# Kernel optimization log

Hardware: AMD Instinct MI355X
Metric: run time of the kernel (lower is better)

Reference implementation:

```python
import jax, jax.numpy as jnp
import numpy as np

D_MODEL = 256
N_FEATURES = 32768
N_BLOCKS = 8
MIN_FEATURES = 512
BATCH = 2048
ALPHA = 0.99          # RunningAvgNormalizer alpha
EPS_CTRL = 3e-4       # L1RegController eps
TARGET_L0 = 100.0


def _pareto_seg(n_features, n_blocks, min_features, rng):
    # mirrors get_pareto_block_bounds, returning per-feature block ids
    cdf = 1.0 - (np.arange(n_features - min_features + 1) / (n_features - min_features + 1)) ** 0.5
    pdf = np.concatenate([np.zeros(min_features), np.abs(cdf[1:] - cdf[:-1])])
    pdf = pdf / pdf.sum()
    sp = np.sort(rng.choice(n_features, size=n_blocks - 1, replace=False, p=pdf))
    return np.searchsorted(sp, np.arange(n_features), side='right').astype(np.int32)


def setup_inputs() -> dict:
    key = jax.random.key(0)
    k0, k1 = jax.random.split(key, 2)
    x = jax.random.normal(k0, (BATCH, D_MODEL), jnp.float32)
    W_enc = jax.random.normal(k1, (D_MODEL, N_FEATURES), jnp.float32) / np.sqrt(D_MODEL)
    b_enc = -0.04 * jnp.ones((N_FEATURES,), jnp.float32)
    W_dec = (0.1 * W_enc / jnp.linalg.norm(W_enc, axis=0, keepdims=True)).T
    b_dec = jnp.zeros((D_MODEL,), jnp.float32)
    bw = np.arange(1, N_BLOCKS + 1, dtype=np.float32) ** 1.0  # block_weight_power = 1.0
    block_weights = jnp.asarray(bw / bw.max())
    running_avg = jnp.asarray([np.sqrt(D_MODEL)], jnp.float32)  # warmed-up running norm
    l1_scale = jnp.ones((1,), jnp.float32)
    seg = jnp.asarray(_pareto_seg(N_FEATURES, N_BLOCKS, MIN_FEATURES, np.random.default_rng(0)))
    return {"x": x, "W_enc": W_enc, "b_enc": b_enc, "W_dec": W_dec, "b_dec": b_dec,
            "block_weights": block_weights, "running_avg": running_avg,
            "l1_scale": l1_scale, "seg": seg}


def reference(x, W_enc, b_enc, W_dec, b_dec, block_weights, running_avg, l1_scale, seg):
    K = block_weights.shape[0]
    B, d = x.shape
    # RunningAvgNormalizer.normalize(update=True): update EMA, then scale (no grad through EMA)
    ra = ALPHA * running_avg[0] + (1.0 - ALPHA) * jnp.mean(jnp.linalg.norm(x, axis=-1))
    ra = jax.lax.stop_gradient(ra)
    xn = x * (jnp.sqrt(jnp.float32(d)) / ra)
    acts = jax.nn.relu(xn @ W_enc + b_enc)                       # [B, F]
    Wd_norms = jnp.linalg.norm(W_dec, axis=1)                    # [F]
    # per-block log-loss: sum over block features of mean-over-batch log term
    per_feat = jnp.mean(jnp.log(acts * Wd_norms + 0.1) - jnp.log(0.1), axis=0)  # [F]
    block_l1 = jax.ops.segment_sum(per_feat, seg, num_segments=K)               # [K]
    l1_loss = jnp.mean(block_weights * jnp.cumsum(block_l1))
    # per-block decode: (acts masked to block) @ W_dec, sequential over K small blocks
    onehot = (seg[None, :] == jnp.arange(K)[:, None]).astype(acts.dtype)  # [K, F]
    block_preds = jax.lax.map(lambda m: (acts * m) @ W_dec, onehot)       # [K, B, d]
    cum_preds = jnp.cumsum(block_preds, axis=0) + b_dec                   # b_dec added to preds[0] pre-cumsum
    block_errs = jnp.mean(jnp.sum((cum_preds - xn[None]) ** 2, axis=-1), axis=-1) * block_weights
    mse_loss = jnp.mean(block_errs)
    # L1RegController (no-grad)
    avg_l0 = jax.lax.stop_gradient(jnp.sum(acts > 0).astype(jnp.float32) / B)
    l1_reg_scale = jnp.where(avg_l0 < TARGET_L0, l1_scale[0] * (1.0 - EPS_CTRL), l1_scale[0] * (1.0 + EPS_CTRL))
    loss = mse_loss + l1_reg_scale * l1_loss
    return loss
```

## Files before the change

kernel.cpp:

```cpp
#include <hip/hip_runtime.h>

typedef float  f32x4  __attribute__((ext_vector_type(4)));
typedef __bf16 bf16x8 __attribute__((ext_vector_type(8)));
typedef __bf16 bf16x4 __attribute__((ext_vector_type(4)));
typedef unsigned short u16;

#define BATCH 2048
#define DM    256
#define NFEAT 32768
#define NBLK  8
#define ALPHA_C   0.99f
#define EPS_CTRL  3e-4f
#define TARGET_L0 100.0f

#define BT    32
#define FC    2048
#define NCHUNK (NFEAT / FC)
#define MACRO 128
#define NMACRO (FC / MACRO)
#define NPMAX 24
#define ACTS_SZ (BT * MACRO)

#define WS_RA    0
#define WS_SCALE 1
#define WS_L0    2
#define WS_L1    4
#define WS_ERR   16
#define WSI_BND  32
#define WSI_PTN  40
#define WSI_PTS  41
#define WSI_PSEG 66
#define WS_WDN   256
#define PIECES_OFF_BYTES ((size_t)262144)
#define PIECES_BYTES ((size_t)NPMAX * BATCH * DM * 2)
#define WEP_OFF_BYTES (PIECES_OFF_BYTES + PIECES_BYTES)
#define WDP_OFF_BYTES (WEP_OFF_BYTES + (size_t)NFEAT * DM * 2)

#define RAW_BARRIER() asm volatile("s_waitcnt lgkmcnt(0)\n\ts_barrier" ::: "memory")

static __device__ inline u16 f2b(float f) {
    return __builtin_bit_cast(u16, (__bf16)f);
}
static __device__ inline float b2f(u16 u) {
    return (float)__builtin_bit_cast(__bf16, u);
}
static __device__ inline f32x4 mfma16(bf16x8 a, bf16x8 b, f32x4 c) {
    return __builtin_amdgcn_mfma_f32_16x16x32_bf16(a, b, c, 0, 0, 0);
}

__global__ __launch_bounds__(256) void k_prep(const float* __restrict__ x,
                                              const float* __restrict__ Wd,
                                              const int* __restrict__ seg,
                                              float* ws) {
    const int bid = blockIdx.x;
    const int wave = threadIdx.x >> 6, lane = threadIdx.x & 63;
    if (bid < NFEAT / 4) {
        const int f = bid * 4 + wave;
        const float4 v = *reinterpret_cast<const float4*>(Wd + (size_t)f * DM + lane * 4);
        float s = v.x * v.x + v.y * v.y + v.z * v.z + v.w * v.w;
        #pragma unroll
        for (int o = 32; o; o >>= 1) s += __shfl_xor(s, o);
        if (lane == 0) ws[WS_WDN + f] = sqrtf(s);
    } else if (bid < NFEAT / 4 + BATCH / 4) {
        const int row = (bid - NFEAT / 4) * 4 + wave;
        const float4 v = *reinterpret_cast<const float4*>(x + (size_t)row * DM + lane * 4);
        float s = v.x * v.x + v.y * v.y + v.z * v.z + v.w * v.w;
        #pragma unroll
        for (int o = 32; o; o >>= 1) s += __shfl_xor(s, o);
        if (lane == 0) atomicAdd(&ws[WS_RA], sqrtf(s));
    } else {
        const int f = (bid - NFEAT / 4 - BATCH / 4) * 256 + threadIdx.x;
        if (f > 0 && f < NFEAT) {
            const int s = seg[f];
            if (s != seg[f - 1]) ((int*)ws)[WSI_BND + s] = f;
        }
    }
}

__global__ void k_pt2(const int* __restrict__ seg,
                      const float* __restrict__ ravg, float* ws) {
    __shared__ int stv[NCHUNK + NBLK];
    __shared__ int outL[NPMAX];
    __shared__ int NL;
    int* wsi = (int*)ws;
    const int t = threadIdx.x;
    if (t < NCHUNK) stv[t] = t * FC;
    else if (t < NCHUNK + NBLK - 1) stv[t] = wsi[WSI_BND + (t - NCHUNK + 1)];
    __syncthreads();
    if (t == 0) {
        int i = 0, j = NCHUNK, N = 0;
        while (i < NCHUNK || j < NCHUNK + NBLK - 1) {
            int v;
            if (i < NCHUNK && (j >= NCHUNK + NBLK - 1 || stv[i] <= stv[j])) v = stv[i++];
            else v = stv[j++];
            if (N == 0 || outL[N - 1] != v) outL[N++] = v;
        }
        NL = N;
    }
    __syncthreads();
    const int N = NL;
    if (t < N) {
        wsi[WSI_PTS + t] = outL[t];
        wsi[WSI_PSEG + t] = seg[outL[t]];
    }
    if (t == 0) {
        wsi[WSI_PTN] = N;
        wsi[WSI_PTS + N] = NFEAT;
        float ra = ALPHA_C * ravg[0] + (1.0f - ALPHA_C) * (ws[WS_RA] / (float)BATCH);
        ws[WS_SCALE] = 16.0f / ra;
    }
}

__global__ __launch_bounds__(256) void k_pack(const float* __restrict__ We,
                                              const float* __restrict__ Wd,
                                              u16* __restrict__ WeP,
                                              u16* __restrict__ WdP) {
    const int bid = blockIdx.x;
    if (bid < 4096) {
        const int tid = bid * 256 + threadIdx.x;
        const int l = tid & 63, kf = (tid >> 6) & 7, F = tid >> 9;
        const int f = F * 16 + (l & 15);
        const int kb = kf * 32 + (l >> 4) * 8;
        bf16x8 v;
        #pragma unroll
        for (int i = 0; i < 8; ++i)
            v[i] = (__bf16)We[(size_t)(kb + i) * NFEAT + f];
        *reinterpret_cast<bf16x8*>(WeP + (size_t)tid * 8) = v;
    } else {
        const int tid = (bid - 4096) * 256 + threadIdx.x;
        const int l = tid & 63, G = (tid >> 6) & 1023, Dg = tid >> 16;
        const int d = Dg * 16 + (l & 15);
        const int fb = G * 32 + (l >> 4) * 8;
        bf16x8 v;
        #pragma unroll
        for (int i = 0; i < 8; ++i)
            v[i] = (__bf16)Wd[(size_t)(fb + i) * DM + d];
        *reinterpret_cast<bf16x8*>(WdP + (size_t)tid * 8) = v;
    }
}

__global__ __launch_bounds__(256, 2) void k_main(const float* __restrict__ x,
                                                 const float* __restrict__ be,
                                                 const int* __restrict__ seg,
                                                 float* __restrict__ ws,
                                                 u16* __restrict__ pieces,
                                                 const u16* __restrict__ WeP,
                                                 const u16* __restrict__ WdP) {
    __shared__ __align__(16) u16 xs[BT * DM];
    __shared__ __align__(16) u16 acts[2 * ACTS_SZ];
    __shared__ int segL[FC];
    __shared__ float lds_l1[NBLK];
    __shared__ unsigned lds_l0;
    __shared__ int s2s[NBLK];
    __shared__ int msegL[NMACRO];
    __shared__ int muniL[NMACRO];

    const int t = threadIdx.x;
    const int w = t >> 6;
    const int l = t & 63;
    const int l15 = l & 15, lg = l >> 4;
    const int f0 = blockIdx.x * FC;
    const int b0 = blockIdx.y * BT;
    const float scale = ws[WS_SCALE];
    const int* wsi = (const int*)ws;

    if (t < NBLK) lds_l1[t] = 0.0f;
    if (t == 0) lds_l0 = 0u;
    if (t < NPMAX) {
        const int N = wsi[WSI_PTN];
        if (t < N) {
            const int ps = wsi[WSI_PTS + t];
            if (ps >= f0 && ps < f0 + FC) s2s[wsi[WSI_PSEG + t]] = t;
        }
    }

    #pragma unroll
    for (int p = 0; p < 2; ++p)
        reinterpret_cast<int4*>(segL)[t + p * 256] =
            reinterpret_cast<const int4*>(seg + f0)[t + p * 256];

    #pragma unroll
    for (int p = 0; p < 8; ++p) {
        const int row = p * 4 + (t >> 6);
        const int col = (t & 63) * 4;
        const float4 v = *reinterpret_cast<const float4*>(x + (size_t)(b0 + row) * DM + col);
        bf16x4 h;
        h[0] = (__bf16)(v.x * scale); h[1] = (__bf16)(v.y * scale);
        h[2] = (__bf16)(v.z * scale); h[3] = (__bf16)(v.w * scale);
        const int e = (((row >> 4) * 8 + (col >> 5)) * 512 + ((col >> 3) & 3) * 128 + (row & 15) * 8 + (col & 7));
        *reinterpret_cast<bf16x4*>(&xs[e]) = h;
    }
    __syncthreads();
    if (t < NMACRO) {
        msegL[t] = segL[t * MACRO];
        muniL[t] = (segL[t * MACRO] == segL[t * MACRO + MACRO - 1]);
    }
    __syncthreads();

    f32x4 pacc[2][4];
    #pragma unroll
    for (int i = 0; i < 2; ++i)
        #pragma unroll
        for (int j = 0; j < 4; ++j) pacc[i][j] = (f32x4)0.0f;

    int cur = msegL[0];
    float l1a0 = 0.0f, l1a1 = 0.0f;
    int myseg = -1;
    unsigned l0c = 0u;
    const int Dg0 = 4 * w;

    auto flush = [&](int s) {
        u16* pb = pieces + (size_t)s2s[s] * (BATCH * DM);
        #pragma unroll
        for (int rt = 0; rt < 2; ++rt)
            #pragma unroll
            for (int ct = 0; ct < 4; ++ct)
                #pragma unroll
                for (int r = 0; r < 4; ++r) {
                    const int row = b0 + 16 * rt + lg * 4 + r;
                    const int col = 64 * w + 16 * ct + l15;
                    pb[(size_t)row * DM + col] = f2b(pacc[rt][ct][r]);
                    pacc[rt][ct][r] = 0.0f;
                }
    };

    auto encodeR = [&](f32x4 (&eacc)[2][2], bf16x8 (&we)[2][8]) {
        #pragma unroll
        for (int kf = 0; kf < 8; ++kf) {
            bf16x8 a[2];
            #pragma unroll
            for (int rt = 0; rt < 2; ++rt)
                a[rt] = *reinterpret_cast<const bf16x8*>(&xs[((rt * 8 + kf) * 64 + l) * 8]);
            #pragma unroll
            for (int rt = 0; rt < 2; ++rt)
                #pragma unroll
                for (int ct = 0; ct < 2; ++ct)
                    eacc[rt][ct] = mfma16(a[rt], we[ct][kf], eacc[rt][ct]);
        }
    };

    auto epilogue = [&](int it, f32x4 (&eacc)[2][2], const float* biasv, const float* wdnv) {
        const bool uni = (muniL[it] != 0);
        u16* ab = acts + (it & 1) * ACTS_SZ;
        const int fbl = it * MACRO;
        #pragma unroll
        for (int ct = 0; ct < 2; ++ct) {
            const int s = uni ? msegL[it] : segL[fbl + 32 * w + 16 * ct + l15];
            if (s != myseg) {
                if (myseg >= 0) atomicAdd(&lds_l1[myseg], l1a0 + l1a1);
                l1a0 = 0.0f; l1a1 = 0.0f; myseg = s;
            }
            #pragma unroll
            for (int rt = 0; rt < 2; ++rt)
                #pragma unroll
                for (int r = 0; r < 4; ++r) {
                    float a = eacc[rt][ct][r] + biasv[ct];
                    a = fmaxf(a, 0.0f);
                    l0c += (unsigned)__popcll(__ballot(a > 0.0f));
                    if (rt == 0) l1a0 += __logf(fmaf(a, wdnv[ct], 1.0f));
                    else         l1a1 += __logf(fmaf(a, wdnv[ct], 1.0f));
                    const int e = (rt * 4 + w) * 512 + (2 * ct + (l15 >> 3)) * 128 + (lg * 4 + r) * 8 + (l15 & 7);
                    ab[e] = f2b(a);
                }
        }
    };

    auto decodeR = [&](int ms, bf16x8 (&wdv)[4][4]) {
        const u16* ab = acts + (ms & 1) * ACTS_SZ;
        if (muniL[ms]) {
            const int s = msegL[ms];
            if (s != cur) { flush(cur); cur = s; }
            #pragma unroll
            for (int kf = 0; kf < 4; ++kf) {
                bf16x8 a[2];
                #pragma unroll
                for (int rt = 0; rt < 2; ++rt)
                    a[rt] = *reinterpret_cast<const bf16x8*>(&ab[((rt * 4 + kf) * 64 + l) * 8]);
                #pragma unroll
                for (int rt = 0; rt < 2; ++rt)
                    #pragma unroll
                    for (int ct = 0; ct < 4; ++ct)
                        pacc[rt][ct] = mfma16(a[rt], wdv[ct][kf], pacc[rt][ct]);
            }
        } else {
            const int fbl = ms * MACRO;
            #pragma unroll
            for (int kf = 0; kf < 4; ++kf) {
                const int W0 = fbl + kf * 32;
                const int s0 = segL[W0], s1 = segL[W0 + 31];
                if (s0 == s1) {
                    if (s0 != cur) { flush(cur); cur = s0; }
                    bf16x8 a[2];
                    #pragma unroll
                    for (int rt = 0; rt < 2; ++rt)
                        a[rt] = *reinterpret_cast<const bf16x8*>(&ab[((rt * 4 + kf) * 64 + l) * 8]);
                    #pragma unroll
                    for (int rt = 0; rt < 2; ++rt)
                        #pragma unroll
                        for (int ct = 0; ct < 4; ++ct)
                            pacc[rt][ct] = mfma16(a[rt], wdv[ct][kf], pacc[rt][ct]);
                } else {
                    int lo = 0;
                    while (lo < 32) {
                        const int s = segL[W0 + lo];
                        int hi = lo + 1;
                        while (hi < 32 && segL[W0 + hi] == s) ++hi;
                        if (s != cur) { flush(cur); cur = s; }
                        bf16x8 a[2];
                        #pragma unroll
                        for (int rt = 0; rt < 2; ++rt) {
                            a[rt] = *reinterpret_cast<const bf16x8*>(&ab[((rt * 4 + kf) * 64 + l) * 8]);
                            #pragma unroll
                            for (int i = 0; i < 8; ++i) {
                                const int kl = lg * 8 + i;
                                if (kl < lo || kl >= hi) a[rt][i] = (__bf16)0.0f;
                            }
                        }
                        #pragma unroll
                        for (int rt = 0; rt < 2; ++rt)
                            #pragma unroll
                            for (int ct = 0; ct < 4; ++ct)
                                pacc[rt][ct] = mfma16(a[rt], wdv[ct][kf], pacc[rt][ct]);
                        lo = hi;
                    }
                }
            }
        }
    };

    {
        bf16x8 we[2][8];
        const int F0 = (f0 >> 4) + 2 * w;
        #pragma unroll
        for (int kf = 0; kf < 8; ++kf)
            #pragma unroll
            for (int ct = 0; ct < 2; ++ct)
                we[ct][kf] = *reinterpret_cast<const bf16x8*>(WeP + (((size_t)(F0 + ct) * 8 + kf) * 64 + l) * 8);
        float biasv[2], wdnv[2];
        #pragma unroll
        for (int ct = 0; ct < 2; ++ct) {
            const int fg = f0 + 32 * w + 16 * ct + l15;
            biasv[ct] = be[fg];
            wdnv[ct] = ws[WS_WDN + fg] * 10.0f;
        }
        f32x4 eacc[2][2];
        #pragma unroll
        for (int i = 0; i < 2; ++i)
            #pragma unroll
            for (int j = 0; j < 2; ++j) eacc[i][j] = (f32x4)0.0f;
        encodeR(eacc, we);
        epilogue(0, eacc, biasv, wdnv);
    }

    for (int it = 1; it <= NMACRO; ++it) {
        RAW_BARRIER();
        const int itm1 = it - 1;

        if (it < NMACRO) {
            bf16x8 we[2][8];
            const int F0 = ((f0 + it * MACRO) >> 4) + 2 * w;
            #pragma unroll
            for (int kf = 0; kf < 8; ++kf)
                #pragma unroll
                for (int ct = 0; ct < 2; ++ct)
                    we[ct][kf] = *reinterpret_cast<const bf16x8*>(WeP + (((size_t)(F0 + ct) * 8 + kf) * 64 + l) * 8);
            bf16x8 wdv[4][4];
            const int G0 = (f0 + itm1 * MACRO) >> 5;
            #pragma unroll
            for (int kf = 0; kf < 4; ++kf)
                #pragma unroll
                for (int ct = 0; ct < 4; ++ct)
                    wdv[ct][kf] = *reinterpret_cast<const bf16x8*>(WdP + (((size_t)(Dg0 + ct) * 1024 + G0 + kf) * 64 + l) * 8);
            float biasv[2], wdnv[2];
            #pragma unroll
            for (int ct = 0; ct < 2; ++ct) {
                const int fg = f0 + it * MACRO + 32 * w + 16 * ct + l15;
                biasv[ct] = be[fg];
                wdnv[ct] = ws[WS_WDN + fg] * 10.0f;
            }

            f32x4 eacc[2][2];
            #pragma unroll
            for (int i = 0; i < 2; ++i)
                #pragma unroll
                for (int j = 0; j < 2; ++j) eacc[i][j] = (f32x4)0.0f;
            encodeR(eacc, we);
            decodeR(itm1, wdv);
            epilogue(it, eacc, biasv, wdnv);
        } else {
            bf16x8 wdv[4][4];
            const int G0 = (f0 + itm1 * MACRO) >> 5;
            #pragma unroll
            for (int kf = 0; kf < 4; ++kf)
                #pragma unroll
                for (int ct = 0; ct < 4; ++ct)
                    wdv[ct][kf] = *reinterpret_cast<const bf16x8*>(WdP + (((size_t)(Dg0 + ct) * 1024 + G0 + kf) * 64 + l) * 8);
            decodeR(itm1, wdv);
        }
    }

    flush(cur);
    if (myseg >= 0) atomicAdd(&lds_l1[myseg], l1a0 + l1a1);
    if (l == 0) atomicAdd(&lds_l0, l0c);
    __syncthreads();
    if (t < NBLK) atomicAdd(&ws[WS_L1 + t], lds_l1[t]);
    if (t == 0) atomicAdd(((unsigned*)ws) + WS_L0, lds_l0);
}


__global__ __launch_bounds__(256) void k_err(const float* __restrict__ x,
                                             const float* __restrict__ bd,
                                             float* ws,
                                             const u16* __restrict__ pieces) {
    const int b = blockIdx.x, t = threadIdx.x;
    const int wave = t >> 6, lane = t & 63;
    const int* wsi = (const int*)ws;
    const int N = wsi[WSI_PTN];
    const float scale = ws[WS_SCALE];
    const float xv = x[(size_t)b * DM + t] * scale;
    float p = bd[t];
    __shared__ float lds[NBLK][4];
    for (int i = 0; i < N; ++i) {
        p += b2f(pieces[(size_t)i * (BATCH * DM) + (size_t)b * DM + t]);
        const int sg = wsi[WSI_PSEG + i];
        const bool end = (i == N - 1) || (wsi[WSI_PSEG + i + 1] != sg);
        if (end) {
            const float d = p - xv;
            float e = d * d;
            #pragma unroll
            for (int o = 32; o; o >>= 1) e += __shfl_xor(e, o);
            if (lane == 0) lds[sg][wave] = e;
        }
    }
    __syncthreads();
    if (t < NBLK) {
        const float s = lds[t][0] + lds[t][1] + lds[t][2] + lds[t][3];
        atomicAdd(&ws[WS_ERR + t], s);
    }
}

__global__ void k_loss(const float* __restrict__ bw,
                       const float* __restrict__ l1s,
                       const float* ws, float* out) {
    float cum = 0.0f, l1 = 0.0f, mse = 0.0f;
    for (int k = 0; k < NBLK; ++k) {
        cum += ws[WS_L1 + k] / (float)BATCH;
        l1 += bw[k] * cum;
        mse += bw[k] * (ws[WS_ERR + k] / (float)BATCH);
    }
    l1 *= (1.0f / NBLK);
    mse *= (1.0f / NBLK);
    const unsigned l0 = ((const unsigned*)ws)[WS_L0];
    const float avg_l0 = (float)l0 / (float)BATCH;
    const float rs = l1s[0] * (avg_l0 < TARGET_L0 ? (1.0f - EPS_CTRL) : (1.0f + EPS_CTRL));
    out[0] = mse + rs * l1;
}


extern "C" void kernel_launch(void* const* d_in, const int* in_sizes, int n_in,
                              void* d_out, int out_size, void* d_ws, size_t ws_size,
                              hipStream_t stream) {
    const float* x    = (const float*)d_in[0];
    const float* We   = (const float*)d_in[1];
    const float* be   = (const float*)d_in[2];
    const float* Wd   = (const float*)d_in[3];
    const float* bd   = (const float*)d_in[4];
    const float* bw   = (const float*)d_in[5];
    const float* ravg = (const float*)d_in[6];
    const float* l1s  = (const float*)d_in[7];
    const int*   seg  = (const int*)d_in[8];
    float* out = (float*)d_out;
    float* ws  = (float*)d_ws;
    u16* pieces = (u16*)((char*)d_ws + PIECES_OFF_BYTES);
    u16* WeP = (u16*)((char*)d_ws + WEP_OFF_BYTES);
    u16* WdP = (u16*)((char*)d_ws + WDP_OFF_BYTES);

    hipMemsetAsync(d_ws, 0, 1024, stream);
    k_prep<<<NFEAT / 4 + BATCH / 4 + NFEAT / 256, 256, 0, stream>>>(x, Wd, seg, ws);
    k_pack<<<8192, 256, 0, stream>>>(We, Wd, WeP, WdP);
    k_pt2<<<1, 64, 0, stream>>>(seg, ravg, ws);
    dim3 g(NFEAT / FC, BATCH / BT);
    k_main<<<g, 256, 0, stream>>>(x, be, seg, ws, pieces, WeP, WdP);
    k_err<<<BATCH, 256, 0, stream>>>(x, bd, ws, pieces);
    k_loss<<<1, 1, 0, stream>>>(bw, l1s, ws, out);
}
```

Baseline: 237.5 us.

## Tile weight packing through LDS, fuse decoder norms, trim seg staging in main

The weight pack kernel now loads coalesced 32-row tiles of W_enc and W_dec into shared memory and transposes them there, replacing strided global gathers. The W_dec row-norm computation moves from the prep kernel into the pack kernel, so W_dec is read once. In the main kernel the per-chunk seg copy in shared memory and one barrier are removed; seg is read from global memory instead. The epilogue is moved before the decode MMA, and the L0 count switches from a per-lane ballot popcount to a plain per-lane counter with per-thread atomics. This trades extra LDS traffic in packing and more global seg reads and shared atomics in main for fewer strided global loads.

```diff
diff --git a/kernel.cpp b/kernel.cpp
--- a/kernel.cpp
+++ b/kernel.cpp
@@ -49,27 +49,19 @@
 }
 
 __global__ __launch_bounds__(256) void k_prep(const float* __restrict__ x,
-                                              const float* __restrict__ Wd,
                                               const int* __restrict__ seg,
                                               float* ws) {
     const int bid = blockIdx.x;
     const int wave = threadIdx.x >> 6, lane = threadIdx.x & 63;
-    if (bid < NFEAT / 4) {
-        const int f = bid * 4 + wave;
-        const float4 v = *reinterpret_cast<const float4*>(Wd + (size_t)f * DM + lane * 4);
-        float s = v.x * v.x + v.y * v.y + v.z * v.z + v.w * v.w;
-        #pragma unroll
-        for (int o = 32; o; o >>= 1) s += __shfl_xor(s, o);
-        if (lane == 0) ws[WS_WDN + f] = sqrtf(s);
-    } else if (bid < NFEAT / 4 + BATCH / 4) {
-        const int row = (bid - NFEAT / 4) * 4 + wave;
+    if (bid < BATCH / 4) {
+        const int row = bid * 4 + wave;
         const float4 v = *reinterpret_cast<const float4*>(x + (size_t)row * DM + lane * 4);
         float s = v.x * v.x + v.y * v.y + v.z * v.z + v.w * v.w;
         #pragma unroll
         for (int o = 32; o; o >>= 1) s += __shfl_xor(s, o);
         if (lane == 0) atomicAdd(&ws[WS_RA], sqrtf(s));
     } else {
-        const int f = (bid - NFEAT / 4 - BATCH / 4) * 256 + threadIdx.x;
+        const int f = (bid - BATCH / 4) * 256 + threadIdx.x;
         if (f > 0 && f < NFEAT) {
             const int s = seg[f];
             if (s != seg[f - 1]) ((int*)ws)[WSI_BND + s] = f;
@@ -114,28 +106,64 @@
 __global__ __launch_bounds__(256) void k_pack(const float* __restrict__ We,
                                               const float* __restrict__ Wd,
                                               u16* __restrict__ WeP,
-                                              u16* __restrict__ WdP) {
+                                              u16* __restrict__ WdP,
+                                              float* ws) {
+    __shared__ float tile[32][261];
+    const int t = threadIdx.x;
     const int bid = blockIdx.x;
-    if (bid < 4096) {
-        const int tid = bid * 256 + threadIdx.x;
-        const int l = tid & 63, kf = (tid >> 6) & 7, F = tid >> 9;
-        const int f = F * 16 + (l & 15);
-        const int kb = kf * 32 + (l >> 4) * 8;
-        bf16x8 v;
-        #pragma unroll
-        for (int i = 0; i < 8; ++i)
-            v[i] = (__bf16)We[(size_t)(kb + i) * NFEAT + f];
-        *reinterpret_cast<bf16x8*>(WeP + (size_t)tid * 8) = v;
+    if (bid < 1024) {
+        const int kf = bid & 7, fblk = bid >> 3;
+        const int f0 = fblk * 256;
+        #pragma unroll
+        for (int p = 0; p < 8; ++p) {
+            const int r = p * 4 + (t >> 6);
+            const int c = (t & 63) * 4;
+            const float4 v = *reinterpret_cast<const float4*>(We + (size_t)(kf * 32 + r) * NFEAT + f0 + c);
+            tile[r][c] = v.x; tile[r][c + 1] = v.y; tile[r][c + 2] = v.z; tile[r][c + 3] = v.w;
+        }
+        __syncthreads();
+        #pragma unroll
+        for (int p = 0; p < 4; ++p) {
+            const int item = p * 256 + t;
+            const int g = item >> 6, l = item & 63;
+            const int F = fblk * 16 + g;
+            bf16x8 v;
+            #pragma unroll
+            for (int i = 0; i < 8; ++i)
+                v[i] = (__bf16)tile[(l >> 4) * 8 + i][g * 16 + (l & 15)];
+            *reinterpret_cast<bf16x8*>(WeP + ((size_t)(F * 8 + kf) * 64 + l) * 8) = v;
+        }
     } else {
-        const int tid = (bid - 4096) * 256 + threadIdx.x;
-        const int l = tid & 63, G = (tid >> 6) & 1023, Dg = tid >> 16;
-        const int d = Dg * 16 + (l & 15);
-        const int fb = G * 32 + (l >> 4) * 8;
-        bf16x8 v;
-        #pragma unroll
-        for (int i = 0; i < 8; ++i)
-            v[i] = (__bf16)Wd[(size_t)(fb + i) * DM + d];
-        *reinterpret_cast<bf16x8*>(WdP + (size_t)tid * 8) = v;
+        const int G = bid - 1024;
+        #pragma unroll
+        for (int p = 0; p < 8; ++p) {
+            const int r = p * 4 + (t >> 6);
+            const int c = (t & 63) * 4;
+            const float4 v = *reinterpret_cast<const float4*>(Wd + (size_t)(G * 32 + r) * DM + c);
+            tile[r][c] = v.x; tile[r][c + 1] = v.y; tile[r][c + 2] = v.z; tile[r][c + 3] = v.w;
+        }
+        __syncthreads();
+        {
+            const int row = t >> 3, part = t & 7;
+            float s = 0.0f;
+            #pragma unroll
+            for (int j = 0; j < 32; ++j) {
+                const float xv = tile[row][part * 32 + j];
+                s += xv * xv;
+            }
+            s += __shfl_xor(s, 1); s += __shfl_xor(s, 2); s += __shfl_xor(s, 4);
+            if (part == 0) ws[WS_WDN + G * 32 + row] = sqrtf(s);
+        }
+        #pragma unroll
+        for (int p = 0; p < 4; ++p) {
+            const int item = p * 256 + t;
+            const int g = item >> 6, l = item & 63;
+            bf16x8 v;
+            #pragma unroll
+            for (int i = 0; i < 8; ++i)
+                v[i] = (__bf16)tile[(l >> 4) * 8 + i][g * 16 + (l & 15)];
+            *reinterpret_cast<bf16x8*>(WdP + ((size_t)(g * 1024 + G) * 64 + l) * 8) = v;
+        }
     }
 }
 
@@ -148,7 +176,6 @@
                                                  const u16* __restrict__ WdP) {
     __shared__ __align__(16) u16 xs[BT * DM];
     __shared__ __align__(16) u16 acts[2 * ACTS_SZ];
-    __shared__ int segL[FC];
     __shared__ float lds_l1[NBLK];
     __shared__ unsigned lds_l0;
     __shared__ int s2s[NBLK];
@@ -173,11 +200,12 @@
             if (ps >= f0 && ps < f0 + FC) s2s[wsi[WSI_PSEG + t]] = t;
         }
     }
-
-    #pragma unroll
-    for (int p = 0; p < 2; ++p)
-        reinterpret_cast<int4*>(segL)[t + p * 256] =
-            reinterpret_cast<const int4*>(seg + f0)[t + p * 256];
+    if (t < NMACRO) {
+        const int a0 = seg[f0 + t * MACRO];
+        const int a1 = seg[f0 + t * MACRO + MACRO - 1];
+        msegL[t] = a0;
+        muniL[t] = (a0 == a1);
+    }
 
     #pragma unroll
     for (int p = 0; p < 8; ++p) {
@@ -191,11 +219,6 @@
         *reinterpret_cast<bf16x4*>(&xs[e]) = h;
     }
     __syncthreads();
-    if (t < NMACRO) {
-        msegL[t] = segL[t * MACRO];
-        muniL[t] = (segL[t * MACRO] == segL[t * MACRO + MACRO - 1]);
-    }
-    __syncthreads();
 
     f32x4 pacc[2][4];
     #pragma unroll
@@ -242,10 +265,10 @@
     auto epilogue = [&](int it, f32x4 (&eacc)[2][2], const float* biasv, const float* wdnv) {
         const bool uni = (muniL[it] != 0);
         u16* ab = acts + (it & 1) * ACTS_SZ;
-        const int fbl = it * MACRO;
         #pragma unroll
         for (int ct = 0; ct < 2; ++ct) {
-            const int s = uni ? msegL[it] : segL[fbl + 32 * w + 16 * ct + l15];
+            const int fg = f0 + it * MACRO + 32 * w + 16 * ct + l15;
+            const int s = uni ? msegL[it] : seg[fg];
             if (s != myseg) {
                 if (myseg >= 0) atomicAdd(&lds_l1[myseg], l1a0 + l1a1);
                 l1a0 = 0.0f; l1a1 = 0.0f; myseg = s;
@@ -256,7 +279,7 @@
                 for (int r = 0; r < 4; ++r) {
                     float a = eacc[rt][ct][r] + biasv[ct];
                     a = fmaxf(a, 0.0f);
-                    l0c += (unsigned)__popcll(__ballot(a > 0.0f));
+                    l0c += (a > 0.0f) ? 1u : 0u;
                     if (rt == 0) l1a0 += __logf(fmaf(a, wdnv[ct], 1.0f));
                     else         l1a1 += __logf(fmaf(a, wdnv[ct], 1.0f));
                     const int e = (rt * 4 + w) * 512 + (2 * ct + (l15 >> 3)) * 128 + (lg * 4 + r) * 8 + (l15 & 7);
@@ -283,11 +306,11 @@
                         pacc[rt][ct] = mfma16(a[rt], wdv[ct][kf], pacc[rt][ct]);
             }
         } else {
-            const int fbl = ms * MACRO;
+            const int fb = f0 + ms * MACRO;
             #pragma unroll
             for (int kf = 0; kf < 4; ++kf) {
-                const int W0 = fbl + kf * 32;
-                const int s0 = segL[W0], s1 = segL[W0 + 31];
+                const int W0 = fb + kf * 32;
+                const int s0 = seg[W0], s1 = seg[W0 + 31];
                 if (s0 == s1) {
                     if (s0 != cur) { flush(cur); cur = s0; }
                     bf16x8 a[2];
@@ -302,9 +325,9 @@
                 } else {
                     int lo = 0;
                     while (lo < 32) {
-                        const int s = segL[W0 + lo];
+                        const int s = seg[W0 + lo];
                         int hi = lo + 1;
-                        while (hi < 32 && segL[W0 + hi] == s) ++hi;
+                        while (hi < 32 && seg[W0 + hi] == s) ++hi;
                         if (s != cur) { flush(cur); cur = s; }
                         bf16x8 a[2];
                         #pragma unroll
@@ -385,8 +408,8 @@
                 #pragma unroll
                 for (int j = 0; j < 2; ++j) eacc[i][j] = (f32x4)0.0f;
             encodeR(eacc, we);
+            epilogue(it, eacc, biasv, wdnv);
             decodeR(itm1, wdv);
-            epilogue(it, eacc, biasv, wdnv);
         } else {
             bf16x8 wdv[4][4];
             const int G0 = (f0 + itm1 * MACRO) >> 5;
@@ -401,7 +424,7 @@
 
     flush(cur);
     if (myseg >= 0) atomicAdd(&lds_l1[myseg], l1a0 + l1a1);
-    if (l == 0) atomicAdd(&lds_l0, l0c);
+    atomicAdd(&lds_l0, l0c);
     __syncthreads();
     if (t < NBLK) atomicAdd(&ws[WS_L1 + t], lds_l1[t]);
     if (t == 0) atomicAdd(((unsigned*)ws) + WS_L0, lds_l0);
@@ -476,8 +499,8 @@
     u16* WdP = (u16*)((char*)d_ws + WDP_OFF_BYTES);
 
     hipMemsetAsync(d_ws, 0, 1024, stream);
-    k_prep<<<NFEAT / 4 + BATCH / 4 + NFEAT / 256, 256, 0, stream>>>(x, Wd, seg, ws);
-    k_pack<<<8192, 256, 0, stream>>>(We, Wd, WeP, WdP);
+    k_prep<<<BATCH / 4 + NFEAT / 256, 256, 0, stream>>>(x, seg, ws);
+    k_pack<<<2048, 256, 0, stream>>>(We, Wd, WeP, WdP, ws);
     k_pt2<<<1, 64, 0, stream>>>(seg, ravg, ws);
     dim3 g(NFEAT / FC, BATCH / BT);
     k_main<<<g, 256, 0, stream>>>(x, be, seg, ws, pieces, WeP, WdP);
```

New measurement: 249.8 us. 1.05x slower.
